# Kernel optimization log

Hardware: AMD Instinct MI355X
Metric: run time of the kernel (lower is better)

## Reference

```python
import jax, jax.numpy as jnp
import numpy as np

SEQ, FEAT = 1048576, 3
IN, HID, OUT = 1, 10, 1

def setup_inputs() -> dict:
    key = jax.random.key(0)
    ks = jax.random.split(key, 7)
    s = 1.0 / np.sqrt(HID)
    return {
        "src": jax.random.normal(ks[0], (SEQ, 1, FEAT), dtype=jnp.float32),
        "W_ih": jax.random.uniform(ks[1], (HID, IN), jnp.float32, -s, s),
        "W_hh": jax.random.uniform(ks[2], (HID, HID), jnp.float32, -s, s),
        "b_ih": jax.random.uniform(ks[3], (HID,), jnp.float32, -s, s),
        "b_hh": jax.random.uniform(ks[4], (HID,), jnp.float32, -s, s),
        "W_fc": jax.random.uniform(ks[5], (OUT, HID), jnp.float32, -s, s),
        "b_fc": jax.random.uniform(ks[6], (OUT,), jnp.float32, -s, s),
    }

def reference(src, W_ih, W_hh, b_ih, b_hh, W_fc, b_fc):
    # src: [S, 1, F]; only channel 0 is fed to the RNN (input_size=1)
    x = src[:, :, 0:1]  # [S, 1, 1]
    b = b_ih + b_hh     # [HID]

    def step(h, x_t):
        # h: [1, HID], x_t: [1, 1]
        h_new = jnp.tanh(x_t @ W_ih.T + h @ W_hh.T + b)
        return h_new, h_new

    h0 = jnp.zeros((1, HID), dtype=src.dtype)
    _, out = jax.lax.scan(step, h0, x)  # out: [S, 1, HID]
    return out @ W_fc.T + b_fc           # [S, 1, OUT]
```

## Files before the change

### kernel.cpp

```cpp
#include <hip/hip_runtime.h>

typedef float v2f __attribute__((ext_vector_type(2)));
typedef float v4f __attribute__((ext_vector_type(4)));

constexpr int SEQ    = 1048576;
constexpr int HID    = 10;
constexpr int CH     = 16;
constexpr int BURN   = 48;
constexpr int NCHUNK = SEQ / CH;
constexpr int TPB    = 256;
constexpr int PH     = (BURN + CH) / 16;
constexpr int NW     = TPB * CH + BURN;
constexpr int NWP    = NW + NW / 16;

__device__ __forceinline__ v2f tanh2(v2f z) {
    v2f zs = z * 2.8853900817779268f;
    float p = __builtin_amdgcn_exp2f(zs.x) + 1.0f;
    float q = __builtin_amdgcn_exp2f(zs.y) + 1.0f;
    float r = __builtin_amdgcn_rcpf(p * q);
    return v2f{fmaf(-2.0f, q * r, 1.0f), fmaf(-2.0f, p * r, 1.0f)};
}

__global__ void __launch_bounds__(256, 1) rnn_chunk_kernel(
    const float* __restrict__ src,
    const float* __restrict__ W_ih,
    const float* __restrict__ W_hh,
    const float* __restrict__ b_ih,
    const float* __restrict__ b_hh,
    const float* __restrict__ W_fc,
    const float* __restrict__ b_fc,
    float* __restrict__ out)
{
    __shared__ float xs[NWP];

    const int tx      = threadIdx.x;
    const int blk     = blockIdx.x;
    const int lane    = tx & 63;
    const int tid     = blk * TPB + tx;
    const int t_begin = tid * CH;
    const int tbase   = blk * TPB * CH;

#pragma unroll
    for (int i = 0; i < (NW + TPB - 1) / TPB; ++i) {
        int u = i * TPB + tx;
        if (u < NW) {
            int t = tbase - BURN + u;
            xs[u + (u >> 4)] = src[3 * (t > 0 ? t : 0)];
        }
    }

    float tW0 = W_hh[lane];
    float tW1 = W_hh[64 + (lane < 36 ? lane : 0)];
    float tIh = W_ih[lane < 10 ? lane : 0];
    float tBi = b_ih[lane < 10 ? lane : 0];
    float tBh = b_hh[lane < 10 ? lane : 0];
    float tFc = W_fc[lane < 10 ? lane : 0];
    auto getW = [&](int idx) {
        return idx < 64 ? __shfl(tW0, idx) : __shfl(tW1, idx - 64);
    };

    v2f whhT[HID][HID/2];
    v2f bb2[HID/2], wih2[HID/2];
    float wfc[HID], h[HID];
#pragma unroll
    for (int j = 0; j < HID; ++j)
#pragma unroll
        for (int p = 0; p < HID/2; ++p)
            whhT[j][p] = v2f{getW((2*p)*HID + j), getW((2*p+1)*HID + j)};
#pragma unroll
    for (int p = 0; p < HID/2; ++p) {
        bb2[p]  = v2f{__shfl(tBi, 2*p)   + __shfl(tBh, 2*p),
                      __shfl(tBi, 2*p+1) + __shfl(tBh, 2*p+1)};
        wih2[p] = v2f{__shfl(tIh, 2*p), __shfl(tIh, 2*p+1)};
    }
#pragma unroll
    for (int i = 0; i < HID; ++i) { wfc[i] = __shfl(tFc, i); h[i] = 0.0f; }
    const float bfc = b_fc[0];

    __syncthreads();

    auto step = [&](float x) {
        const v2f x2 = v2f{x, x};
        v2f acc[HID/2];
#pragma unroll
        for (int p = 0; p < HID/2; ++p)
            acc[p] = __builtin_elementwise_fma(wih2[p], x2, bb2[p]);
#pragma unroll
        for (int j = 0; j < HID; ++j) {
            const v2f hj2 = v2f{h[j], h[j]};
#pragma unroll
            for (int p = 0; p < HID/2; ++p)
                acc[p] = __builtin_elementwise_fma(whhT[j][p], hj2, acc[p]);
        }
#pragma unroll
        for (int p = 0; p < HID/2; ++p) {
            v2f t2 = tanh2(acc[p]);
            h[2*p] = t2.x; h[2*p+1] = t2.y;
        }
    };

#pragma unroll 1
    for (int ph = 0; ph < PH; ++ph) {
        const int pb = 17 * (tx + ph);
        float xr[16];
#pragma unroll
        for (int k = 0; k < 16; ++k) xr[k] = xs[pb + k];

        const int  tb     = t_begin - BURN + ph * 16;
        const bool emitph = (ph == PH - 1);
        float orr[16];
#pragma unroll
        for (int k = 0; k < 16; ++k) {
            if (tb + k >= 0) {
                step(xr[k]);
                if (emitph) {
                    float o = bfc;
#pragma unroll
                    for (int i = 0; i < HID; ++i) o = fmaf(wfc[i], h[i], o);
                    orr[k] = o;
                }
            }
        }
        if (emitph) {
            v4f* op = (v4f*)(out + t_begin);
#pragma unroll
            for (int q = 0; q < 4; ++q)
                op[q] = v4f{orr[4*q], orr[4*q+1], orr[4*q+2], orr[4*q+3]};
        }
    }
}

extern "C" void kernel_launch(void* const* d_in, const int* in_sizes, int n_in,
                              void* d_out, int out_size, void* d_ws, size_t ws_size,
                              hipStream_t stream) {
    const float* src  = (const float*)d_in[0];
    const float* W_ih = (const float*)d_in[1];
    const float* W_hh = (const float*)d_in[2];
    const float* b_ih = (const float*)d_in[3];
    const float* b_hh = (const float*)d_in[4];
    const float* W_fc = (const float*)d_in[5];
    const float* b_fc = (const float*)d_in[6];
    float* out = (float*)d_out;

    dim3 grid(NCHUNK / TPB);
    dim3 block(TPB);
    rnn_chunk_kernel<<<grid, block, 0, stream>>>(src, W_ih, W_hh, b_ih, b_hh,
                                                 W_fc, b_fc, out);
}
```

Measured before the change: 92.71 us.

## Split each chunk's hidden state across a lane pair with xor shuffles

Each sequence chunk is now handled by two adjacent threads, each owning five of the ten hidden units, and the partner's half of the state is exchanged by __shfl_xor after every step. The output projection is also split in two and reduced with one shuffle. Per-thread work and register use drop, and the launch bound allows two blocks per CU for more occupancy. In exchange the grid doubles, every step adds five cross-lane shuffles to the serial dependency chain, and the burn-in recurrence now runs twice as many threads in total.

```diff
diff --git a/kernel.cpp b/kernel.cpp
--- a/kernel.cpp
+++ b/kernel.cpp
@@ -3,25 +3,31 @@
 typedef float v2f __attribute__((ext_vector_type(2)));
 typedef float v4f __attribute__((ext_vector_type(4)));
 
-constexpr int SEQ    = 1048576;
-constexpr int HID    = 10;
-constexpr int CH     = 16;
-constexpr int BURN   = 48;
-constexpr int NCHUNK = SEQ / CH;
-constexpr int TPB    = 256;
-constexpr int PH     = (BURN + CH) / 16;
-constexpr int NW     = TPB * CH + BURN;
-constexpr int NWP    = NW + NW / 16;
+constexpr int SEQ  = 1048576;
+constexpr int HID  = 10;
+constexpr int CH   = 16;
+constexpr int BURN = 48;
+constexpr int NCH  = SEQ / CH;
+constexpr int TPB  = 256;
+constexpr int CPB  = TPB / 2;
+constexpr int PH   = (BURN + CH) / 16;
+constexpr int NW   = CPB * CH + BURN;
+constexpr int NWP  = NW + NW / 16 + 1;
 
-__device__ __forceinline__ v2f tanh2(v2f z) {
+__device__ __forceinline__ void tanh2(v2f z, float& o0, float& o1) {
     v2f zs = z * 2.8853900817779268f;
     float p = __builtin_amdgcn_exp2f(zs.x) + 1.0f;
     float q = __builtin_amdgcn_exp2f(zs.y) + 1.0f;
     float r = __builtin_amdgcn_rcpf(p * q);
-    return v2f{fmaf(-2.0f, q * r, 1.0f), fmaf(-2.0f, p * r, 1.0f)};
+    o0 = fmaf(-2.0f, q * r, 1.0f);
+    o1 = fmaf(-2.0f, p * r, 1.0f);
+}
+__device__ __forceinline__ float tanh1(float z) {
+    float p = __builtin_amdgcn_exp2f(z * 2.8853900817779268f) + 1.0f;
+    return fmaf(-2.0f, __builtin_amdgcn_rcpf(p), 1.0f);
 }
 
-__global__ void __launch_bounds__(256, 1) rnn_chunk_kernel(
+__global__ void __launch_bounds__(256, 2) rnn_pair_kernel(
     const float* __restrict__ src,
     const float* __restrict__ W_ih,
     const float* __restrict__ W_hh,
@@ -34,11 +40,12 @@
     __shared__ float xs[NWP];
 
     const int tx      = threadIdx.x;
+    const int s       = tx & 1;
+    const int cl      = tx >> 1;
     const int blk     = blockIdx.x;
-    const int lane    = tx & 63;
-    const int tid     = blk * TPB + tx;
-    const int t_begin = tid * CH;
-    const int tbase   = blk * TPB * CH;
+    const int pair    = blk * CPB + cl;
+    const int t_begin = pair * CH;
+    const int tbase   = blk * CPB * CH;
 
 #pragma unroll
     for (int i = 0; i < (NW + TPB - 1) / TPB; ++i) {
@@ -49,59 +56,63 @@
         }
     }
 
-    float tW0 = W_hh[lane];
-    float tW1 = W_hh[64 + (lane < 36 ? lane : 0)];
-    float tIh = W_ih[lane < 10 ? lane : 0];
-    float tBi = b_ih[lane < 10 ? lane : 0];
-    float tBh = b_hh[lane < 10 ? lane : 0];
-    float tFc = W_fc[lane < 10 ? lane : 0];
-    auto getW = [&](int idx) {
-        return idx < 64 ? __shfl(tW0, idx) : __shfl(tW1, idx - 64);
-    };
+    const int mu = s * 5;
+    const int pu = 5 - mu;
+    v2f wsA[5], wsB[5], wpA[5], wpB[5];
+    float wsS[5], wpS[5];
+#pragma unroll
+    for (int q = 0; q < 5; ++q) {
+        wsA[q] = v2f{W_hh[(mu+0)*HID + mu+q], W_hh[(mu+1)*HID + mu+q]};
+        wsB[q] = v2f{W_hh[(mu+2)*HID + mu+q], W_hh[(mu+3)*HID + mu+q]};
+        wsS[q] =     W_hh[(mu+4)*HID + mu+q];
+        wpA[q] = v2f{W_hh[(mu+0)*HID + pu+q], W_hh[(mu+1)*HID + pu+q]};
+        wpB[q] = v2f{W_hh[(mu+2)*HID + pu+q], W_hh[(mu+3)*HID + pu+q]};
+        wpS[q] =     W_hh[(mu+4)*HID + pu+q];
+    }
+    v2f   bbA = v2f{b_ih[mu+0] + b_hh[mu+0], b_ih[mu+1] + b_hh[mu+1]};
+    v2f   bbB = v2f{b_ih[mu+2] + b_hh[mu+2], b_ih[mu+3] + b_hh[mu+3]};
+    float bbS = b_ih[mu+4] + b_hh[mu+4];
+    v2f   wiA = v2f{W_ih[mu+0], W_ih[mu+1]};
+    v2f   wiB = v2f{W_ih[mu+2], W_ih[mu+3]};
+    float wiS = W_ih[mu+4];
+    float wf0 = W_fc[mu+0], wf1 = W_fc[mu+1], wf2 = W_fc[mu+2],
+          wf3 = W_fc[mu+3], wf4 = W_fc[mu+4];
+    const float bfc = b_fc[0];
 
-    v2f whhT[HID][HID/2];
-    v2f bb2[HID/2], wih2[HID/2];
-    float wfc[HID], h[HID];
-#pragma unroll
-    for (int j = 0; j < HID; ++j)
-#pragma unroll
-        for (int p = 0; p < HID/2; ++p)
-            whhT[j][p] = v2f{getW((2*p)*HID + j), getW((2*p+1)*HID + j)};
-#pragma unroll
-    for (int p = 0; p < HID/2; ++p) {
-        bb2[p]  = v2f{__shfl(tBi, 2*p)   + __shfl(tBh, 2*p),
-                      __shfl(tBi, 2*p+1) + __shfl(tBh, 2*p+1)};
-        wih2[p] = v2f{__shfl(tIh, 2*p), __shfl(tIh, 2*p+1)};
-    }
-#pragma unroll
-    for (int i = 0; i < HID; ++i) { wfc[i] = __shfl(tFc, i); h[i] = 0.0f; }
-    const float bfc = b_fc[0];
+    float hS[5] = {0,0,0,0,0};
+    float hP[5] = {0,0,0,0,0};
 
     __syncthreads();
 
     auto step = [&](float x) {
         const v2f x2 = v2f{x, x};
-        v2f acc[HID/2];
+        v2f  aA = __builtin_elementwise_fma(wiA, x2, bbA);
+        v2f  aB = __builtin_elementwise_fma(wiB, x2, bbB);
+        float aS = fmaf(wiS, x, bbS);
 #pragma unroll
-        for (int p = 0; p < HID/2; ++p)
-            acc[p] = __builtin_elementwise_fma(wih2[p], x2, bb2[p]);
-#pragma unroll
-        for (int j = 0; j < HID; ++j) {
-            const v2f hj2 = v2f{h[j], h[j]};
-#pragma unroll
-            for (int p = 0; p < HID/2; ++p)
-                acc[p] = __builtin_elementwise_fma(whhT[j][p], hj2, acc[p]);
+        for (int q = 0; q < 5; ++q) {
+            const v2f hq = v2f{hS[q], hS[q]};
+            aA = __builtin_elementwise_fma(wsA[q], hq, aA);
+            aB = __builtin_elementwise_fma(wsB[q], hq, aB);
+            aS = fmaf(wsS[q], hS[q], aS);
         }
 #pragma unroll
-        for (int p = 0; p < HID/2; ++p) {
-            v2f t2 = tanh2(acc[p]);
-            h[2*p] = t2.x; h[2*p+1] = t2.y;
+        for (int q = 0; q < 5; ++q) {
+            const v2f hq = v2f{hP[q], hP[q]};
+            aA = __builtin_elementwise_fma(wpA[q], hq, aA);
+            aB = __builtin_elementwise_fma(wpB[q], hq, aB);
+            aS = fmaf(wpS[q], hP[q], aS);
         }
+        tanh2(aA, hS[0], hS[1]);
+        tanh2(aB, hS[2], hS[3]);
+        hS[4] = tanh1(aS);
+#pragma unroll
+        for (int q = 0; q < 5; ++q) hP[q] = __shfl_xor(hS[q], 1);
     };
 
 #pragma unroll 1
     for (int ph = 0; ph < PH; ++ph) {
-        const int pb = 17 * (tx + ph);
+        const int pb = 17 * (cl + ph);
         float xr[16];
 #pragma unroll
         for (int k = 0; k < 16; ++k) xr[k] = xs[pb + k];
@@ -114,14 +125,14 @@
             if (tb + k >= 0) {
                 step(xr[k]);
                 if (emitph) {
-                    float o = bfc;
-#pragma unroll
-                    for (int i = 0; i < HID; ++i) o = fmaf(wfc[i], h[i], o);
-                    orr[k] = o;
+                    float o = fmaf(wf0, hS[0], fmaf(wf1, hS[1],
+                              fmaf(wf2, hS[2], fmaf(wf3, hS[3], wf4 * hS[4]))));
+                    o += __shfl_xor(o, 1);
+                    orr[k] = o + bfc;
                 }
             }
         }
-        if (emitph) {
+        if (emitph && s == 0) {
             v4f* op = (v4f*)(out + t_begin);
 #pragma unroll
             for (int q = 0; q < 4; ++q)
@@ -142,8 +153,8 @@
     const float* b_fc = (const float*)d_in[6];
     float* out = (float*)d_out;
 
-    dim3 grid(NCHUNK / TPB);
+    dim3 grid(NCH / CPB);
     dim3 block(TPB);
-    rnn_chunk_kernel<<<grid, block, 0, stream>>>(src, W_ih, W_hh, b_ih, b_hh,
-                                                 W_fc, b_fc, out);
+    rnn_pair_kernel<<<grid, block, 0, stream>>>(src, W_ih, W_hh, b_ih, b_hh,
+                                                W_fc, b_fc, out);
 }
```

New measurement: 94.04 us. Within noise of the previous version (+1.4%).
